# Kernel optimization log

Measured on AMD Instinct MI355X. Metric: run time of the kernel, lower is better.

The kernel has to match this reference:

```python
import jax, jax.numpy as jnp
import numpy as np

D = 128      # embedding_dim
E = 50000    # positive edges per metapath
S = 16       # negative samples per edge
N_A = 100000 # nodes of type A (head type of both metapaths)
N_B = 50000  # nodes of type B (tail type of metapath 1)


def setup_inputs() -> dict:
    key = jax.random.key(0)
    ks = jax.random.split(key, 10)
    emb_A = jax.random.normal(ks[0], (N_A, D), dtype=jnp.float32)
    emb_B = jax.random.normal(ks[1], (N_B, D), dtype=jnp.float32)
    # nn.init.uniform_(a=-1, b=1)
    rel_emb = jax.random.uniform(ks[2], (2, D, D), dtype=jnp.float32, minval=-1.0, maxval=1.0)
    edge_index_m0 = jax.random.randint(ks[3], (2, E), 0, N_A)  # A -> A
    edge_index_m1 = jnp.stack([
        jax.random.randint(ks[4], (E,), 0, N_A),               # heads: type A
        jax.random.randint(ks[5], (E,), 0, N_B),               # tails: type B
    ])
    neg_head_m0 = jax.random.randint(ks[6], (E, S), 0, N_A)
    neg_head_m1 = jax.random.randint(ks[7], (E, S), 0, N_A)
    neg_tail_m0 = jax.random.randint(ks[8], (E, S), 0, N_A)
    neg_tail_m1 = jax.random.randint(ks[9], (E, S), 0, N_B)
    return dict(emb_A=emb_A, emb_B=emb_B, rel_emb=rel_emb,
                edge_index_m0=edge_index_m0, edge_index_m1=edge_index_m1,
                neg_head_m0=neg_head_m0, neg_head_m1=neg_head_m1,
                neg_tail_m0=neg_tail_m0, neg_tail_m1=neg_tail_m1)


# The torch module computes score = (A K B^T).sum(dim=1); summing the [E,E]
# score matrix over dim 1 equals contracting with sum_j b_j, so we never
# materialize the [E,E] (or [E*S, E*S]) matrix -- same math, fused reduction.

def _pos_score(K, emb_h, emb_t, edge_index):
    s = emb_t[edge_index[1]].sum(0)          # [d] = sum_j b_j
    return emb_h[edge_index[0]] @ (K @ s)    # [E]


def _neg_head_score(K, emb_h, neg):
    # predict(mode='head'): emb_A = emb_h[neg.reshape(-1)],
    # idx_B = edge_index[0][arange(E)*S] == neg[:, 0],
    # side_B = (K @ emb_h[idx_B].T).repeat_interleave(S, -1); sum over columns
    # == K @ (S * sum_j emb_h[neg[j, 0]]).
    s = neg.shape[1]
    c = K @ (s * emb_h[neg[:, 0]].sum(0))    # [d]
    return emb_h[neg.reshape(-1)] @ c        # [E*S]


def _neg_tail_score(K, emb_t, neg):
    # predict(mode='tail'): emb_B = emb_t[neg.reshape(-1)],
    # idx_A = edge_index[1][arange(E)*S] == neg[:, 0],
    # side_A = (emb_t[idx_A] @ K).repeat_interleave(S, 0); row sums of
    # side_A @ emb_B^T == side_A @ sum_j emb_B[j].
    s = neg.shape[1]
    sb = emb_t[neg.reshape(-1)].sum(0)       # [d]
    base = (emb_t[neg[:, 0]] @ K) @ sb       # [E]
    return jnp.repeat(base, s)               # [E*S]


def reference(emb_A, emb_B, rel_emb, edge_index_m0, edge_index_m1,
              neg_head_m0, neg_head_m1, neg_tail_m0, neg_tail_m1):
    K0, K1 = rel_emb[0], rel_emb[1]
    pos0 = _pos_score(K0, emb_A, emb_A, edge_index_m0)   # [E]
    pos1 = _pos_score(K1, emb_A, emb_B, edge_index_m1)   # [E]
    nh0 = _neg_head_score(K0, emb_A, neg_head_m0)        # [E*S]
    nh1 = _neg_head_score(K1, emb_A, neg_head_m1)        # [E*S]
    nt0 = _neg_tail_score(K0, emb_A, neg_tail_m0)        # [E*S]
    nt1 = _neg_tail_score(K1, emb_B, neg_tail_m1)        # [E*S]
    return jnp.concatenate([pos0, pos1, nh0, nh1, nt0, nt1])
```

## Files before the change

kernel.cpp:

```cpp
#include <hip/hip_runtime.h>
#include <stdint.h>

#define D 128
#define E_EDGES 50000
#define S_NEG 16
#define N_A 100000
#define N_B 50000
#define ES (E_EDGES * S_NEG)

#define CHUNK 12500
#define B_SLABS 68
#define GA 512
#define GB 256
#define RPG 25
#define RA 16
#define RB 8

__device__ inline float dot4(float4 a, float4 b) {
    return a.x * b.x + a.y * b.y + a.z * b.z + a.w * b.w;
}
#define RED32(p) { p += __shfl_xor(p, 1); p += __shfl_xor(p, 2); p += __shfl_xor(p, 4); \
                   p += __shfl_xor(p, 8); p += __shfl_xor(p, 16); }


__global__ void k_hist(const int* __restrict__ ei0, const int* __restrict__ ei1,
                       const int* __restrict__ nh0, const int* __restrict__ nh1,
                       const int* __restrict__ nt0, const int* __restrict__ nt1,
                       uint32_t* __restrict__ partA, uint32_t* __restrict__ partB) {
    __shared__ uint32_t h[CHUNK];
    const int tid = threadIdx.x;
    for (int w = tid; w < CHUNK; w += 256) h[w] = 0;
    __syncthreads();

    const int b = blockIdx.x;
    const int* src; long long base; int stride, lo; uint32_t* dst;
    if (b < 8) {
        const int c = b >> 1, hh = b & 1;
        src = ei0; base = E_EDGES + (long long)c * CHUNK; stride = 1;
        lo = hh * 50000; dst = partA + (size_t)(c * 2 + hh) * CHUNK;
    } else if (b < 16) {
        const int q = b - 8, c = q >> 1, hh = q & 1;
        src = nh0; base = (long long)c * CHUNK * S_NEG; stride = S_NEG;
        lo = hh * 50000; dst = partA + (size_t)((4 + c) * 2 + hh) * CHUNK;
    } else if (b < 24) {
        const int q = b - 16, c = q >> 1, hh = q & 1;
        src = nh1; base = (long long)c * CHUNK * S_NEG; stride = S_NEG;
        lo = hh * 50000; dst = partA + (size_t)((8 + c) * 2 + hh) * CHUNK;
    } else if (b < 152) {
        const int q = b - 24, c = q >> 1, hh = q & 1;
        src = nt0; base = (long long)c * CHUNK; stride = 1;
        lo = hh * 50000; dst = partA + (size_t)((12 + c) * 2 + hh) * CHUNK;
    } else if (b < 156) {
        const int c = b - 152;
        src = ei1; base = E_EDGES + (long long)c * CHUNK; stride = 1;
        lo = 0; dst = partB + (size_t)c * CHUNK;
    } else {
        const int c = b - 156;
        src = nt1; base = (long long)c * CHUNK; stride = 1;
        lo = 0; dst = partB + (size_t)(4 + c) * CHUNK;
    }

    for (int i = tid; i < CHUNK; i += 256) {
        const unsigned r = (unsigned)(src[base + (long long)i * stride] - lo);
        if (r < 50000u) atomicAdd(&h[r >> 2], 1u << ((r & 3u) * 8u));
    }
    __syncthreads();
    for (int w = tid; w < CHUNK; w += 256) dst[w] = h[w];
}

__global__ void k_reduceC(const uint32_t* __restrict__ partA,
                          const uint32_t* __restrict__ partB,
                          float4* __restrict__ cwA, float2* __restrict__ cwB) {
    const int t = blockIdx.x * 256 + threadIdx.x;
    if (t < N_A) {
        const int n = t;
        const int hh = (n >= 50000);
        const int w = (n - hh * 50000) >> 2;
        const int sh = (n & 3) * 8;
        const uint32_t* p = partA + (size_t)hh * CHUNK + w;
        unsigned s0 = 0, s1 = 0, s2 = 0, s3 = 0;
#pragma unroll
        for (int c = 0; c < 4; ++c)   s0 += (p[(size_t)(c * 2) * CHUNK] >> sh) & 255u;
#pragma unroll
        for (int c = 4; c < 8; ++c)   s1 += (p[(size_t)(c * 2) * CHUNK] >> sh) & 255u;
#pragma unroll
        for (int c = 8; c < 12; ++c)  s2 += (p[(size_t)(c * 2) * CHUNK] >> sh) & 255u;
#pragma unroll 8
        for (int c = 12; c < 76; ++c) s3 += (p[(size_t)(c * 2) * CHUNK] >> sh) & 255u;
        cwA[n] = make_float4((float)s0, (float)s1, (float)s2, (float)s3);
    } else if (t < N_A + N_B) {
        const int n = t - N_A;
        const int w = n >> 2;
        const int sh = (n & 3) * 8;
        const uint32_t* p = partB + w;
        unsigned s0 = 0, s1 = 0;
#pragma unroll
        for (int c = 0; c < 4; ++c)   s0 += (p[(size_t)c * CHUNK] >> sh) & 255u;
#pragma unroll 8
        for (int c = 4; c < 68; ++c)  s1 += (p[(size_t)c * CHUNK] >> sh) & 255u;
        cwB[n] = make_float2((float)s0, (float)s1);
    }
}

__global__ void k_scan1(const float* __restrict__ embA, const float* __restrict__ embB,
                        const float4* __restrict__ cwA, const float2* __restrict__ cwB,
                        float* __restrict__ psumA, float* __restrict__ psumB) {
    __shared__ float sds[4 * D];
    const int tid = threadIdx.x;
    const int l = tid & 31;
    const int grp = tid >> 5;

    for (int j = tid; j < 4 * D; j += 256) sds[j] = 0.f;
    __syncthreads();

    if ((int)blockIdx.x < GA) {
        const int gid = blockIdx.x * 8 + grp;
        int r = gid * RPG;
        const int end = min(r + RPG, N_A);
        float acc[16];
#pragma unroll
        for (int k = 0; k < 16; ++k) acc[k] = 0.f;
        const float* base = embA + 4 * l;
        for (; r + 4 <= end; r += 4) {
            float4 w[4], x[4];
#pragma unroll
            for (int u = 0; u < 4; ++u) w[u] = cwA[r + u];
#pragma unroll
            for (int u = 0; u < 4; ++u)
                x[u] = *reinterpret_cast<const float4*>(base + (size_t)(r + u) * D);
#pragma unroll
            for (int u = 0; u < 4; ++u) {
                acc[0]  += w[u].x * x[u].x; acc[1]  += w[u].x * x[u].y;
                acc[2]  += w[u].x * x[u].z; acc[3]  += w[u].x * x[u].w;
                acc[4]  += w[u].y * x[u].x; acc[5]  += w[u].y * x[u].y;
                acc[6]  += w[u].y * x[u].z; acc[7]  += w[u].y * x[u].w;
                acc[8]  += w[u].z * x[u].x; acc[9]  += w[u].z * x[u].y;
                acc[10] += w[u].z * x[u].z; acc[11] += w[u].z * x[u].w;
                acc[12] += w[u].w * x[u].x; acc[13] += w[u].w * x[u].y;
                acc[14] += w[u].w * x[u].z; acc[15] += w[u].w * x[u].w;
            }
        }
        for (; r < end; ++r) {
            const float4 w0 = cwA[r];
            const float4 x0 = *reinterpret_cast<const float4*>(base + (size_t)r * D);
            acc[0]  += w0.x * x0.x; acc[1]  += w0.x * x0.y; acc[2]  += w0.x * x0.z; acc[3]  += w0.x * x0.w;
            acc[4]  += w0.y * x0.x; acc[5]  += w0.y * x0.y; acc[6]  += w0.y * x0.z; acc[7]  += w0.y * x0.w;
            acc[8]  += w0.z * x0.x; acc[9]  += w0.z * x0.y; acc[10] += w0.z * x0.z; acc[11] += w0.z * x0.w;
            acc[12] += w0.w * x0.x; acc[13] += w0.w * x0.y; acc[14] += w0.w * x0.z; acc[15] += w0.w * x0.w;
        }
#pragma unroll
        for (int p = 0; p < 4; ++p)
#pragma unroll
            for (int k = 0; k < 4; ++k)
                atomicAdd(&sds[p * D + 4 * l + k], acc[p * 4 + k]);
        __syncthreads();
        for (int j = tid; j < 4 * D; j += 256)
            psumA[(size_t)blockIdx.x * 512 + j] = sds[j];
    } else {
        const int gid = (blockIdx.x - GA) * 8 + grp;
        int r = gid * RPG;
        const int end = min(r + RPG, N_B);
        float acc[8];
#pragma unroll
        for (int k = 0; k < 8; ++k) acc[k] = 0.f;
        const float* base = embB + 4 * l;
        for (; r + 4 <= end; r += 4) {
            float2 w[4]; float4 x[4];
#pragma unroll
            for (int u = 0; u < 4; ++u) w[u] = cwB[r + u];
#pragma unroll
            for (int u = 0; u < 4; ++u)
                x[u] = *reinterpret_cast<const float4*>(base + (size_t)(r + u) * D);
#pragma unroll
            for (int u = 0; u < 4; ++u) {
                acc[0] += w[u].x * x[u].x; acc[1] += w[u].x * x[u].y;
                acc[2] += w[u].x * x[u].z; acc[3] += w[u].x * x[u].w;
                acc[4] += w[u].y * x[u].x; acc[5] += w[u].y * x[u].y;
                acc[6] += w[u].y * x[u].z; acc[7] += w[u].y * x[u].w;
            }
        }
        for (; r < end; ++r) {
            const float2 w0 = cwB[r];
            const float4 x0 = *reinterpret_cast<const float4*>(base + (size_t)r * D);
            acc[0] += w0.x * x0.x; acc[1] += w0.x * x0.y; acc[2] += w0.x * x0.z; acc[3] += w0.x * x0.w;
            acc[4] += w0.y * x0.x; acc[5] += w0.y * x0.y; acc[6] += w0.y * x0.z; acc[7] += w0.y * x0.w;
        }
#pragma unroll
        for (int p = 0; p < 2; ++p)
#pragma unroll
            for (int k = 0; k < 4; ++k)
                atomicAdd(&sds[p * D + 4 * l + k], acc[p * 4 + k]);
        __syncthreads();
        for (int j = tid; j < 2 * D; j += 256)
            psumB[(size_t)(blockIdx.x - GA) * 256 + j] = sds[j];
    }
}

__global__ void k_red1(const float* __restrict__ psumA, const float* __restrict__ psumB,
                       float* __restrict__ psumA2, float* __restrict__ psumB2) {
    const int b = blockIdx.x, t = threadIdx.x;
    if (b < RA) {
        const float* p = psumA + (size_t)b * 32 * 512;
        float s0 = 0.f, s1 = 0.f;
#pragma unroll 8
        for (int r = 0; r < 32; ++r) { s0 += p[r * 512 + t]; s1 += p[r * 512 + 256 + t]; }
        psumA2[(size_t)b * 512 + t] = s0;
        psumA2[(size_t)b * 512 + 256 + t] = s1;
    } else {
        const int bi = b - RA;
        const float* p = psumB + (size_t)bi * 32 * 256;
        float s = 0.f;
#pragma unroll 8
        for (int r = 0; r < 32; ++r) s += p[r * 256 + t];
        psumB2[(size_t)bi * 256 + t] = s;
    }
}

__global__ void k_cvec2(const float* __restrict__ rel,
                        const float* __restrict__ psumA2, const float* __restrict__ psumB2,
                        float* __restrict__ cvec) {
    const int j = blockIdx.x;
    const int tid = threadIdx.x;
    __shared__ float Kds[D * 129];
    __shared__ float red[256];
    __shared__ float sv[D];
    const float* Kp = rel + (size_t)(j & 1) * D * D;

    for (int e = tid; e < D * D / 4; e += 256) {
        const int row = e >> 5, col = (e & 31) * 4;
        const float4 v = *reinterpret_cast<const float4*>(Kp + (size_t)row * D + col);
        float* dst = Kds + row * 129 + col;
        dst[0] = v.x; dst[1] = v.y; dst[2] = v.z; dst[3] = v.w;
    }

    const int g = tid >> 7, i = tid & 127;
    float s = 0.f;
    if (j == 1 || j == 5) {
        const int plane = (j == 1) ? 0 : 1;
        for (int b = g; b < RB; b += 2) s += psumB2[(size_t)b * 256 + plane * D + i];
    } else {
        const int plane = (j == 0) ? 0 : (j - 1);
        for (int b = g; b < RA; b += 2) s += psumA2[(size_t)b * 512 + plane * D + i];
    }
    red[tid] = s;
    __syncthreads();
    if (tid < 128) sv[i] = red[i] + red[128 + i];
    __syncthreads();

    if (tid < 128) {
        const float scale = (j == 2 || j == 3) ? (float)S_NEG : 1.0f;
        float acc = 0.f;
#pragma unroll
        for (int k = 0; k < D; k += 4)
            acc += Kds[i * 129 + k] * sv[k] + Kds[i * 129 + k + 1] * sv[k + 1]
                 + Kds[i * 129 + k + 2] * sv[k + 2] + Kds[i * 129 + k + 3] * sv[k + 3];
        cvec[j * D + i] = acc * scale;
    }
}

__global__ void k_scan2(const float* __restrict__ embA, const float* __restrict__ embB,
                        const float* __restrict__ cvec, float* __restrict__ PA,
                        float* __restrict__ PB) {
    __shared__ float sc[5 * D];
    const int tid = threadIdx.x;
    const int l = tid & 31;
    const int grp = tid >> 5;

    if ((int)blockIdx.x < GA) {
        for (int j = tid; j < 5 * D; j += 256) sc[j] = cvec[j];
        __syncthreads();
        float4 cf[5];
#pragma unroll
        for (int p = 0; p < 5; ++p)
            cf[p] = *reinterpret_cast<const float4*>(sc + p * D + 4 * l);
        const int gid = blockIdx.x * 8 + grp;
        int r = gid * RPG;
        const int end = min(r + RPG, N_A);
        const float* base = embA + 4 * l;
        for (; r + 4 <= end; r += 4) {
            float4 x[4];
#pragma unroll
            for (int u = 0; u < 4; ++u)
                x[u] = *reinterpret_cast<const float4*>(base + (size_t)(r + u) * D);
            float p_[4][5];
#pragma unroll
            for (int u = 0; u < 4; ++u)
#pragma unroll
                for (int p = 0; p < 5; ++p) p_[u][p] = dot4(x[u], cf[p]);
#pragma unroll
            for (int u = 0; u < 4; ++u)
#pragma unroll
                for (int p = 0; p < 5; ++p) RED32(p_[u][p]);
            if (l < 4) {
                float* o = PA + (size_t)(r + l) * 5;
#pragma unroll
                for (int p = 0; p < 5; ++p)
                    o[p] = (l == 1) ? p_[1][p] : (l == 2) ? p_[2][p] : (l == 3) ? p_[3][p] : p_[0][p];
            }
        }
        for (; r < end; ++r) {
            const float4 x0 = *reinterpret_cast<const float4*>(base + (size_t)r * D);
            float q[5];
#pragma unroll
            for (int p = 0; p < 5; ++p) { q[p] = dot4(x0, cf[p]); RED32(q[p]); }
            if (l == 0) {
                float* o = PA + (size_t)r * 5;
#pragma unroll
                for (int p = 0; p < 5; ++p) o[p] = q[p];
            }
        }
    } else {
        for (int j = tid; j < D; j += 256) sc[j] = cvec[5 * D + j];
        __syncthreads();
        const float4 cf = *reinterpret_cast<const float4*>(sc + 4 * l);
        const int gid = (blockIdx.x - GA) * 8 + grp;
        int r = gid * RPG;
        const int end = min(r + RPG, N_B);
        const float* base = embB + 4 * l;
        for (; r + 4 <= end; r += 4) {
            float4 x[4];
#pragma unroll
            for (int u = 0; u < 4; ++u)
                x[u] = *reinterpret_cast<const float4*>(base + (size_t)(r + u) * D);
            float p_[4];
#pragma unroll
            for (int u = 0; u < 4; ++u) { p_[u] = dot4(x[u], cf); RED32(p_[u]); }
            if (l < 4)
                PB[r + l] = (l == 1) ? p_[1] : (l == 2) ? p_[2] : (l == 3) ? p_[3] : p_[0];
        }
        for (; r < end; ++r) {
            const float4 x0 = *reinterpret_cast<const float4*>(base + (size_t)r * D);
            float q = dot4(x0, cf); RED32(q);
            if (l == 0) PB[r] = q;
        }
    }
}

__global__ void k_scatter(const int* __restrict__ ei0, const int* __restrict__ ei1,
                          const int* __restrict__ nh0, const int* __restrict__ nh1,
                          const int* __restrict__ nt0, const int* __restrict__ nt1,
                          const float* __restrict__ PA, const float* __restrict__ PB,
                          float* __restrict__ out) {
    const int total4 = (2 * E_EDGES + 4 * ES) / 4;
    for (int t = blockIdx.x * blockDim.x + threadIdx.x; t < total4;
         t += gridDim.x * blockDim.x) {
        const int e = t * 4;
        float4 v;
        if (e < E_EDGES) {
            const int4 i4 = *reinterpret_cast<const int4*>(ei0 + e);
            v = make_float4(PA[(size_t)i4.x * 5], PA[(size_t)i4.y * 5],
                            PA[(size_t)i4.z * 5], PA[(size_t)i4.w * 5]);
        } else if (e < 2 * E_EDGES) {
            const int4 i4 = *reinterpret_cast<const int4*>(ei1 + (e - E_EDGES));
            v = make_float4(PA[(size_t)i4.x * 5 + 1], PA[(size_t)i4.y * 5 + 1],
                            PA[(size_t)i4.z * 5 + 1], PA[(size_t)i4.w * 5 + 1]);
        } else if (e < 2 * E_EDGES + ES) {
            const int4 i4 = *reinterpret_cast<const int4*>(nh0 + (e - 2 * E_EDGES));
            v = make_float4(PA[(size_t)i4.x * 5 + 2], PA[(size_t)i4.y * 5 + 2],
                            PA[(size_t)i4.z * 5 + 2], PA[(size_t)i4.w * 5 + 2]);
        } else if (e < 2 * E_EDGES + 2 * ES) {
            const int4 i4 = *reinterpret_cast<const int4*>(nh1 + (e - 2 * E_EDGES - ES));
            v = make_float4(PA[(size_t)i4.x * 5 + 3], PA[(size_t)i4.y * 5 + 3],
                            PA[(size_t)i4.z * 5 + 3], PA[(size_t)i4.w * 5 + 3]);
        } else if (e < 2 * E_EDGES + 3 * ES) {
            const int i = e - 2 * E_EDGES - 2 * ES;
            const float s = PA[(size_t)nt0[(i >> 4) << 4] * 5 + 4];
            v = make_float4(s, s, s, s);
        } else {
            const int i = e - 2 * E_EDGES - 3 * ES;
            const float s = PB[nt1[(i >> 4) << 4]];
            v = make_float4(s, s, s, s);
        }
        *reinterpret_cast<float4*>(out + e) = v;
    }
}

extern "C" void kernel_launch(void* const* d_in, const int* in_sizes, int n_in,
                              void* d_out, int out_size, void* d_ws, size_t ws_size,
                              hipStream_t stream) {
    const float* embA = (const float*)d_in[0];
    const float* embB = (const float*)d_in[1];
    const float* rel  = (const float*)d_in[2];
    const int* ei0 = (const int*)d_in[3];
    const int* ei1 = (const int*)d_in[4];
    const int* nh0 = (const int*)d_in[5];
    const int* nh1 = (const int*)d_in[6];
    const int* nt0 = (const int*)d_in[7];
    const int* nt1 = (const int*)d_in[8];
    float* out = (float*)d_out;

    uint32_t* partA = (uint32_t*)d_ws;
    uint32_t* partB = partA + (size_t)152 * CHUNK;
    float4* cwA = (float4*)(partB + (size_t)B_SLABS * CHUNK);
    float2* cwB = (float2*)(cwA + N_A);
    float* psumA = (float*)(cwB + N_B);
    float* psumB = psumA + (size_t)GA * 512;
    float* psumA2 = psumB + (size_t)GB * 256;
    float* psumB2 = psumA2 + (size_t)RA * 512;
    float* cvec  = psumB2 + (size_t)RB * 256;
    float* PA    = cvec + 6 * D;
    float* PB    = PA + (size_t)N_A * 5;

    k_hist<<<220, 256, 0, stream>>>(ei0, ei1, nh0, nh1, nt0, nt1, partA, partB);
    k_reduceC<<<(N_A + N_B + 255) / 256, 256, 0, stream>>>(partA, partB, cwA, cwB);
    k_scan1<<<GA + GB, 256, 0, stream>>>(embA, embB, cwA, cwB, psumA, psumB);
    k_red1<<<RA + RB, 256, 0, stream>>>(psumA, psumB, psumA2, psumB2);
    k_cvec2<<<6, 256, 0, stream>>>(rel, psumA2, psumB2, cvec);
    k_scan2<<<GA + GB, 256, 0, stream>>>(embA, embB, cvec, PA, PB);
    k_scatter<<<2048, 256, 0, stream>>>(ei0, ei1, nh0, nh1, nt0, nt1, PA, PB, out);
}
```

Measured before the change: 214.7 us.

## Rework histogram chunking, double scan grids, and store projections column-major

The histogram kernel now runs 512-thread blocks, each over 25000 indices instead of 12500, and reads contiguous index streams as int4. This halves the number of partial histograms that must be written and then reduced. The scan kernels get twice as many blocks with fewer rows per group. The per-node projection array PA moves from interleaved [N,5] to planar [5,N], so each scatter gather reads one contiguous plane. The risks are fewer hist blocks, meaning less parallelism, and a larger partial-sum reduction in the scan stage.

```diff
diff --git a/kernel.cpp b/kernel.cpp
--- a/kernel.cpp
+++ b/kernel.cpp
@@ -8,13 +8,14 @@
 #define N_B 50000
 #define ES (E_EDGES * S_NEG)
 
-#define CHUNK 12500
-#define B_SLABS 68
-#define GA 512
-#define GB 256
-#define RPG 25
-#define RA 16
-#define RB 8
+#define HW 12500
+#define ACH 38
+#define BCH 34
+#define GA 1024
+#define GB 512
+#define RPG 13
+#define RA 32
+#define RB 16
 
 __device__ inline float dot4(float4 a, float4 b) {
     return a.x * b.x + a.y * b.y + a.z * b.z + a.w * b.w;
@@ -27,45 +28,55 @@
                        const int* __restrict__ nh0, const int* __restrict__ nh1,
                        const int* __restrict__ nt0, const int* __restrict__ nt1,
                        uint32_t* __restrict__ partA, uint32_t* __restrict__ partB) {
-    __shared__ uint32_t h[CHUNK];
+    __shared__ uint32_t h[HW];
     const int tid = threadIdx.x;
-    for (int w = tid; w < CHUNK; w += 256) h[w] = 0;
+    for (int w = tid; w < HW; w += 512) h[w] = 0;
     __syncthreads();
 
     const int b = blockIdx.x;
-    const int* src; long long base; int stride, lo; uint32_t* dst;
-    if (b < 8) {
+    if (b < 2 * ACH) {
         const int c = b >> 1, hh = b & 1;
-        src = ei0; base = E_EDGES + (long long)c * CHUNK; stride = 1;
-        lo = hh * 50000; dst = partA + (size_t)(c * 2 + hh) * CHUNK;
-    } else if (b < 16) {
-        const int q = b - 8, c = q >> 1, hh = q & 1;
-        src = nh0; base = (long long)c * CHUNK * S_NEG; stride = S_NEG;
-        lo = hh * 50000; dst = partA + (size_t)((4 + c) * 2 + hh) * CHUNK;
-    } else if (b < 24) {
-        const int q = b - 16, c = q >> 1, hh = q & 1;
-        src = nh1; base = (long long)c * CHUNK * S_NEG; stride = S_NEG;
-        lo = hh * 50000; dst = partA + (size_t)((8 + c) * 2 + hh) * CHUNK;
-    } else if (b < 152) {
-        const int q = b - 24, c = q >> 1, hh = q & 1;
-        src = nt0; base = (long long)c * CHUNK; stride = 1;
-        lo = hh * 50000; dst = partA + (size_t)((12 + c) * 2 + hh) * CHUNK;
-    } else if (b < 156) {
-        const int c = b - 152;
-        src = ei1; base = E_EDGES + (long long)c * CHUNK; stride = 1;
-        lo = 0; dst = partB + (size_t)c * CHUNK;
+        const unsigned lo = hh * 50000u;
+        uint32_t* dst = partA + (size_t)b * HW;
+        if (c >= 2 && c < 6) {
+            const int* src = (c < 4) ? nh0 : nh1;
+            const long long base = (long long)(c & 1) * 25000 * S_NEG;
+            for (int i = tid; i < 25000; i += 512) {
+                const unsigned r = (unsigned)src[base + (long long)i * S_NEG] - lo;
+                if (r < 50000u) atomicAdd(&h[r >> 2], 1u << ((r & 3u) * 8u));
+            }
+        } else {
+            const int* srcp = (c < 2) ? (ei0 + E_EDGES + c * 25000)
+                                      : (nt0 + (c - 6) * 25000);
+            const int4* src4 = reinterpret_cast<const int4*>(srcp);
+            for (int i = tid; i < 6250; i += 512) {
+                const int4 v = src4[i];
+                unsigned r;
+                r = (unsigned)v.x - lo; if (r < 50000u) atomicAdd(&h[r >> 2], 1u << ((r & 3u) * 8u));
+                r = (unsigned)v.y - lo; if (r < 50000u) atomicAdd(&h[r >> 2], 1u << ((r & 3u) * 8u));
+                r = (unsigned)v.z - lo; if (r < 50000u) atomicAdd(&h[r >> 2], 1u << ((r & 3u) * 8u));
+                r = (unsigned)v.w - lo; if (r < 50000u) atomicAdd(&h[r >> 2], 1u << ((r & 3u) * 8u));
+            }
+        }
+        __syncthreads();
+        for (int w = tid; w < HW; w += 512) dst[w] = h[w];
     } else {
-        const int c = b - 156;
-        src = nt1; base = (long long)c * CHUNK; stride = 1;
-        lo = 0; dst = partB + (size_t)(4 + c) * CHUNK;
-    }
-
-    for (int i = tid; i < CHUNK; i += 256) {
-        const unsigned r = (unsigned)(src[base + (long long)i * stride] - lo);
-        if (r < 50000u) atomicAdd(&h[r >> 2], 1u << ((r & 3u) * 8u));
-    }
-    __syncthreads();
-    for (int w = tid; w < CHUNK; w += 256) dst[w] = h[w];
+        const int c = b - 2 * ACH;
+        uint32_t* dst = partB + (size_t)c * HW;
+        const int* srcp = (c < 2) ? (ei1 + E_EDGES + c * 25000)
+                                  : (nt1 + (c - 2) * 25000);
+        const int4* src4 = reinterpret_cast<const int4*>(srcp);
+        for (int i = tid; i < 6250; i += 512) {
+            const int4 v = src4[i];
+            unsigned r;
+            r = (unsigned)v.x; if (r < 50000u) atomicAdd(&h[r >> 2], 1u << ((r & 3u) * 8u));
+            r = (unsigned)v.y; if (r < 50000u) atomicAdd(&h[r >> 2], 1u << ((r & 3u) * 8u));
+            r = (unsigned)v.z; if (r < 50000u) atomicAdd(&h[r >> 2], 1u << ((r & 3u) * 8u));
+            r = (unsigned)v.w; if (r < 50000u) atomicAdd(&h[r >> 2], 1u << ((r & 3u) * 8u));
+        }
+        __syncthreads();
+        for (int w = tid; w < HW; w += 512) dst[w] = h[w];
+    }
 }
 
 __global__ void k_reduceC(const uint32_t* __restrict__ partA,
@@ -77,16 +88,16 @@
         const int hh = (n >= 50000);
         const int w = (n - hh * 50000) >> 2;
         const int sh = (n & 3) * 8;
-        const uint32_t* p = partA + (size_t)hh * CHUNK + w;
+        const uint32_t* p = partA + (size_t)hh * HW + w;
         unsigned s0 = 0, s1 = 0, s2 = 0, s3 = 0;
 #pragma unroll
-        for (int c = 0; c < 4; ++c)   s0 += (p[(size_t)(c * 2) * CHUNK] >> sh) & 255u;
-#pragma unroll
-        for (int c = 4; c < 8; ++c)   s1 += (p[(size_t)(c * 2) * CHUNK] >> sh) & 255u;
-#pragma unroll
-        for (int c = 8; c < 12; ++c)  s2 += (p[(size_t)(c * 2) * CHUNK] >> sh) & 255u;
+        for (int c = 0; c < 2; ++c)  s0 += (p[(size_t)(c * 2) * HW] >> sh) & 255u;
+#pragma unroll
+        for (int c = 2; c < 4; ++c)  s1 += (p[(size_t)(c * 2) * HW] >> sh) & 255u;
+#pragma unroll
+        for (int c = 4; c < 6; ++c)  s2 += (p[(size_t)(c * 2) * HW] >> sh) & 255u;
 #pragma unroll 8
-        for (int c = 12; c < 76; ++c) s3 += (p[(size_t)(c * 2) * CHUNK] >> sh) & 255u;
+        for (int c = 6; c < 38; ++c) s3 += (p[(size_t)(c * 2) * HW] >> sh) & 255u;
         cwA[n] = make_float4((float)s0, (float)s1, (float)s2, (float)s3);
     } else if (t < N_A + N_B) {
         const int n = t - N_A;
@@ -95,9 +106,9 @@
         const uint32_t* p = partB + w;
         unsigned s0 = 0, s1 = 0;
 #pragma unroll
-        for (int c = 0; c < 4; ++c)   s0 += (p[(size_t)c * CHUNK] >> sh) & 255u;
+        for (int c = 0; c < 2; ++c)  s0 += (p[(size_t)c * HW] >> sh) & 255u;
 #pragma unroll 8
-        for (int c = 4; c < 68; ++c)  s1 += (p[(size_t)c * CHUNK] >> sh) & 255u;
+        for (int c = 2; c < 34; ++c) s1 += (p[(size_t)c * HW] >> sh) & 255u;
         cwB[n] = make_float2((float)s0, (float)s1);
     }
 }
@@ -292,10 +303,14 @@
 #pragma unroll
                 for (int p = 0; p < 5; ++p) RED32(p_[u][p]);
             if (l < 4) {
-                float* o = PA + (size_t)(r + l) * 5;
-#pragma unroll
-                for (int p = 0; p < 5; ++p)
-                    o[p] = (l == 1) ? p_[1][p] : (l == 2) ? p_[2][p] : (l == 3) ? p_[3][p] : p_[0][p];
+#pragma unroll
+                for (int p = 0; p < 5; ++p) {
+                    float v = p_[0][p];
+                    v = (l == 1) ? p_[1][p] : v;
+                    v = (l == 2) ? p_[2][p] : v;
+                    v = (l == 3) ? p_[3][p] : v;
+                    PA[(size_t)p * N_A + r + l] = v;
+                }
             }
         }
         for (; r < end; ++r) {
@@ -304,9 +319,8 @@
 #pragma unroll
             for (int p = 0; p < 5; ++p) { q[p] = dot4(x0, cf[p]); RED32(q[p]); }
             if (l == 0) {
-                float* o = PA + (size_t)r * 5;
-#pragma unroll
-                for (int p = 0; p < 5; ++p) o[p] = q[p];
+#pragma unroll
+                for (int p = 0; p < 5; ++p) PA[(size_t)p * N_A + r] = q[p];
             }
         }
     } else {
@@ -342,29 +356,30 @@
                           const float* __restrict__ PA, const float* __restrict__ PB,
                           float* __restrict__ out) {
     const int total4 = (2 * E_EDGES + 4 * ES) / 4;
+    const float* P0 = PA;
+    const float* P1 = PA + (size_t)N_A;
+    const float* P2 = PA + (size_t)2 * N_A;
+    const float* P3 = PA + (size_t)3 * N_A;
+    const float* P4 = PA + (size_t)4 * N_A;
     for (int t = blockIdx.x * blockDim.x + threadIdx.x; t < total4;
          t += gridDim.x * blockDim.x) {
         const int e = t * 4;
         float4 v;
         if (e < E_EDGES) {
             const int4 i4 = *reinterpret_cast<const int4*>(ei0 + e);
-            v = make_float4(PA[(size_t)i4.x * 5], PA[(size_t)i4.y * 5],
-                            PA[(size_t)i4.z * 5], PA[(size_t)i4.w * 5]);
+            v = make_float4(P0[i4.x], P0[i4.y], P0[i4.z], P0[i4.w]);
         } else if (e < 2 * E_EDGES) {
             const int4 i4 = *reinterpret_cast<const int4*>(ei1 + (e - E_EDGES));
-            v = make_float4(PA[(size_t)i4.x * 5 + 1], PA[(size_t)i4.y * 5 + 1],
-                            PA[(size_t)i4.z * 5 + 1], PA[(size_t)i4.w * 5 + 1]);
+            v = make_float4(P1[i4.x], P1[i4.y], P1[i4.z], P1[i4.w]);
         } else if (e < 2 * E_EDGES + ES) {
             const int4 i4 = *reinterpret_cast<const int4*>(nh0 + (e - 2 * E_EDGES));
-            v = make_float4(PA[(size_t)i4.x * 5 + 2], PA[(size_t)i4.y * 5 + 2],
-                            PA[(size_t)i4.z * 5 + 2], PA[(size_t)i4.w * 5 + 2]);
+            v = make_float4(P2[i4.x], P2[i4.y], P2[i4.z], P2[i4.w]);
         } else if (e < 2 * E_EDGES + 2 * ES) {
             const int4 i4 = *reinterpret_cast<const int4*>(nh1 + (e - 2 * E_EDGES - ES));
-            v = make_float4(PA[(size_t)i4.x * 5 + 3], PA[(size_t)i4.y * 5 + 3],
-                            PA[(size_t)i4.z * 5 + 3], PA[(size_t)i4.w * 5 + 3]);
+            v = make_float4(P3[i4.x], P3[i4.y], P3[i4.z], P3[i4.w]);
         } else if (e < 2 * E_EDGES + 3 * ES) {
             const int i = e - 2 * E_EDGES - 2 * ES;
-            const float s = PA[(size_t)nt0[(i >> 4) << 4] * 5 + 4];
+            const float s = P4[nt0[(i >> 4) << 4]];
             v = make_float4(s, s, s, s);
         } else {
             const int i = e - 2 * E_EDGES - 3 * ES;
@@ -390,8 +405,8 @@
     float* out = (float*)d_out;
 
     uint32_t* partA = (uint32_t*)d_ws;
-    uint32_t* partB = partA + (size_t)152 * CHUNK;
-    float4* cwA = (float4*)(partB + (size_t)B_SLABS * CHUNK);
+    uint32_t* partB = partA + (size_t)2 * ACH * HW;
+    float4* cwA = (float4*)(partB + (size_t)BCH * HW);
     float2* cwB = (float2*)(cwA + N_A);
     float* psumA = (float*)(cwB + N_B);
     float* psumB = psumA + (size_t)GA * 512;
@@ -399,9 +414,9 @@
     float* psumB2 = psumA2 + (size_t)RA * 512;
     float* cvec  = psumB2 + (size_t)RB * 256;
     float* PA    = cvec + 6 * D;
-    float* PB    = PA + (size_t)N_A * 5;
-
-    k_hist<<<220, 256, 0, stream>>>(ei0, ei1, nh0, nh1, nt0, nt1, partA, partB);
+    float* PB    = PA + (size_t)5 * N_A;
+
+    k_hist<<<2 * ACH + BCH, 512, 0, stream>>>(ei0, ei1, nh0, nh1, nt0, nt1, partA, partB);
     k_reduceC<<<(N_A + N_B + 255) / 256, 256, 0, stream>>>(partA, partB, cwA, cwB);
     k_scan1<<<GA + GB, 256, 0, stream>>>(embA, embB, cwA, cwB, psumA, psumB);
     k_red1<<<RA + RB, 256, 0, stream>>>(psumA, psumB, psumA2, psumB2);
```

Result: slower. 227.4 us (+5.9%).
